# Kernel optimization log

Measured on AMD Instinct MI355X. Metric: run time of the kernel, lower is better.

The kernel has to match this reference:

```python
import jax, jax.numpy as jnp
import numpy as np

N_NODES = 10000
N_EDGES = 640000
D_FEAT = 128


def setup_inputs() -> dict:
    key = jax.random.key(0)
    k1, k2, k3, k4 = jax.random.split(key, 4)
    edge_feat = jax.random.normal(k1, (N_EDGES, D_FEAT), dtype=jnp.float32)
    node_feat = jax.random.normal(k2, (N_NODES, D_FEAT), dtype=jnp.float32)
    recv_idx = jax.random.randint(k3, (N_EDGES,), 0, N_NODES, dtype=jnp.int64 if jax.config.jax_enable_x64 else jnp.int32)
    W = jax.random.normal(k4, (2 * D_FEAT, D_FEAT), dtype=jnp.float32) * (1.0 / np.sqrt(2 * D_FEAT))
    b = jnp.zeros((D_FEAT,), dtype=jnp.float32)
    return {"edge_feat": edge_feat, "node_feat": node_feat, "recv_idx": recv_idx, "W": W, "b": b}


def reference(edge_feat, node_feat, recv_idx, W, b):
    # Unsorted segment sum: scatter-add edge features into receiver nodes. [E,d] -> [N,d]
    n_nodes = node_feat.shape[0]
    agg = jax.ops.segment_sum(edge_feat, recv_idx, num_segments=n_nodes)
    # Concat node features with aggregated received-edge features. [N, 2d]
    collected = jnp.concatenate([node_feat, agg], axis=-1)
    # node_model: Linear(2d -> d)
    return collected @ W + b
```

## Files before the change

### kernel.cpp

```cpp
#include <hip/hip_runtime.h>

#define N_NODES 10000
#define N_EDGES 640000
#define D_FEAT 128

#define WS_COUNTS 0
#define WS_BSUM   10240
#define WS_BOFF   10304
#define WS_START  16384
#define WS_CURSOR 32768
#define WS_SORTED 49152
#define WS_AGG    689152

#define NPB 40

__global__ void zero_counts_kernel(int* __restrict__ counts) {
    int i = blockIdx.x * blockDim.x + threadIdx.x;
    if (i < N_NODES) counts[i] = 0;
}

__global__ void hist_kernel(const int4* __restrict__ recv4, int* __restrict__ counts) {
    int i = blockIdx.x * blockDim.x + threadIdx.x;
    if (i < N_EDGES / 4) {
        const int4 r = recv4[i];
        atomicAdd(&counts[r.x], 1);
        atomicAdd(&counts[r.y], 1);
        atomicAdd(&counts[r.z], 1);
        atomicAdd(&counts[r.w], 1);
    }
}

__global__ __launch_bounds__(256) void prefix1_kernel(const int* __restrict__ counts,
                                                      int* __restrict__ bsum) {
    __shared__ int wsum[4];
    const int tid = threadIdx.x;
    const int idx = blockIdx.x * 256 + tid;
    int x = (idx < N_NODES) ? counts[idx] : 0;
    #pragma unroll
    for (int off = 32; off >= 1; off >>= 1) x += __shfl_down(x, off, 64);
    if ((tid & 63) == 0) wsum[tid >> 6] = x;
    __syncthreads();
    if (tid == 0) bsum[blockIdx.x] = wsum[0] + wsum[1] + wsum[2] + wsum[3];
}

__global__ void prefix2_kernel(const int* __restrict__ bsum,
                               int* __restrict__ boff,
                               int* __restrict__ start) {
    const int lane = threadIdx.x;
    const int v = (lane < NPB) ? bsum[lane] : 0;
    int x = v;
    #pragma unroll
    for (int off = 1; off < 64; off <<= 1) {
        int t = __shfl_up(x, off, 64);
        if (lane >= off) x += t;
    }
    if (lane < NPB) boff[lane] = x - v;
    if (lane == 0) start[N_NODES] = N_EDGES;
}

__global__ __launch_bounds__(256) void prefix3_kernel(const int* __restrict__ counts,
                                                      const int* __restrict__ boff,
                                                      int* __restrict__ start,
                                                      int* __restrict__ cursor) {
    __shared__ int wsum[4];
    const int tid  = threadIdx.x;
    const int idx  = blockIdx.x * 256 + tid;
    const int lane = tid & 63;
    const int wave = tid >> 6;
    const int v = (idx < N_NODES) ? counts[idx] : 0;
    int x = v;
    #pragma unroll
    for (int off = 1; off < 64; off <<= 1) {
        int t = __shfl_up(x, off, 64);
        if (lane >= off) x += t;
    }
    if (lane == 63) wsum[wave] = x;
    __syncthreads();
    int woff = 0;
    #pragma unroll
    for (int k = 0; k < 3; ++k) woff += (k < wave) ? wsum[k] : 0;
    const int excl = boff[blockIdx.x] + woff + x - v;
    if (idx < N_NODES) { start[idx] = excl; cursor[idx] = excl; }
}

__global__ void reorder_kernel(const int4* __restrict__ recv4,
                               int* __restrict__ cursor,
                               int* __restrict__ sorted_eid) {
    int i = blockIdx.x * blockDim.x + threadIdx.x;
    if (i < N_EDGES / 4) {
        const int4 r = recv4[i];
        const int e = i * 4;
        sorted_eid[atomicAdd(&cursor[r.x], 1)] = e + 0;
        sorted_eid[atomicAdd(&cursor[r.y], 1)] = e + 1;
        sorted_eid[atomicAdd(&cursor[r.z], 1)] = e + 2;
        sorted_eid[atomicAdd(&cursor[r.w], 1)] = e + 3;
    }
}

#define GW 16
__global__ __launch_bounds__(512) void gather_kernel(
        const float4* __restrict__ edge_feat4,
        const int* __restrict__ sorted_eid,
        const int* __restrict__ start,
        float4* __restrict__ agg4) {
    __shared__ float4 red[GW][32];
    const int n   = blockIdx.x;
    const int tid = threadIdx.x;
    const int l   = tid & 31;
    const int w   = tid >> 5;
    const int s = start[n];
    const int e = start[n + 1];
    float4 acc = {0.f, 0.f, 0.f, 0.f};
    int i = s + w;
    if (i < e) {
        int eid = sorted_eid[i];
        while (true) {
            const int inext = i + GW;
            const int eid_next = (inext < e) ? sorted_eid[inext] : 0;
            const float4 v = edge_feat4[(long)eid * 32 + l];
            acc.x += v.x; acc.y += v.y; acc.z += v.z; acc.w += v.w;
            i = inext;
            if (i >= e) break;
            eid = eid_next;
        }
    }
    red[w][l] = acc;
    __syncthreads();
    if (w == 0) {
        float4 r = red[0][l];
        #pragma unroll
        for (int g = 1; g < GW; ++g) {
            const float4 t = red[g][l];
            r.x += t.x; r.y += t.y; r.z += t.z; r.w += t.w;
        }
        agg4[(long)n * 32 + l] = r;
    }
}

__global__ __launch_bounds__(256) void gemm_kernel(
        const float* __restrict__ node_feat,
        const float* __restrict__ agg,
        const float* __restrict__ W,
        const float* __restrict__ b,
        float* __restrict__ out) {
    __shared__ __align__(16) float As[32][68];
    __shared__ __align__(16) float Bs[32][64];
    const int tid = threadIdx.x;
    const int tx = tid & 15;
    const int ty = tid >> 4;
    const int m0 = blockIdx.x * 64;
    const int n0 = blockIdx.y * 64;

    float acc[4][4] = {};

    for (int kt = 0; kt < 2 * D_FEAT; kt += 32) {
        const float* src = (kt < D_FEAT) ? (node_feat + kt) : (agg + (kt - D_FEAT));
        {
            const int r  = tid >> 3;
            const int c4 = tid & 7;
            #pragma unroll
            for (int p = 0; p < 2; ++p) {
                int row = m0 + p * 32 + r;
                row = (row < N_NODES) ? row : (N_NODES - 1);
                const float4 a4 = *(const float4*)(src + (long)row * D_FEAT + c4 * 4);
                As[c4 * 4 + 0][p * 32 + r] = a4.x;
                As[c4 * 4 + 1][p * 32 + r] = a4.y;
                As[c4 * 4 + 2][p * 32 + r] = a4.z;
                As[c4 * 4 + 3][p * 32 + r] = a4.w;
            }
        }
        {
            const int r  = tid >> 4;
            const int c4 = tid & 15;
            #pragma unroll
            for (int p = 0; p < 2; ++p) {
                const int row = kt + p * 16 + r;
                *(float4*)&Bs[p * 16 + r][c4 * 4] =
                    *(const float4*)(W + (long)row * D_FEAT + n0 + c4 * 4);
            }
        }
        __syncthreads();
        #pragma unroll
        for (int kk = 0; kk < 32; ++kk) {
            const float4 a4 = *(const float4*)&As[kk][ty * 4];
            const float4 b4 = *(const float4*)&Bs[kk][tx * 4];
            acc[0][0] += a4.x * b4.x; acc[0][1] += a4.x * b4.y;
            acc[0][2] += a4.x * b4.z; acc[0][3] += a4.x * b4.w;
            acc[1][0] += a4.y * b4.x; acc[1][1] += a4.y * b4.y;
            acc[1][2] += a4.y * b4.z; acc[1][3] += a4.y * b4.w;
            acc[2][0] += a4.z * b4.x; acc[2][1] += a4.z * b4.y;
            acc[2][2] += a4.z * b4.z; acc[2][3] += a4.z * b4.w;
            acc[3][0] += a4.w * b4.x; acc[3][1] += a4.w * b4.y;
            acc[3][2] += a4.w * b4.z; acc[3][3] += a4.w * b4.w;
        }
        __syncthreads();
    }

    const float4 bias = *(const float4*)(b + n0 + tx * 4);
    #pragma unroll
    for (int i2 = 0; i2 < 4; ++i2) {
        const int row = m0 + ty * 4 + i2;
        if (row < N_NODES) {
            float4 o;
            o.x = acc[i2][0] + bias.x;
            o.y = acc[i2][1] + bias.y;
            o.z = acc[i2][2] + bias.z;
            o.w = acc[i2][3] + bias.w;
            *(float4*)(out + (long)row * D_FEAT + n0 + tx * 4) = o;
        }
    }
}

extern "C" void kernel_launch(void* const* d_in, const int* in_sizes, int n_in,
                              void* d_out, int out_size, void* d_ws, size_t ws_size,
                              hipStream_t stream) {
    const float* edge_feat = (const float*)d_in[0];
    const float* node_feat = (const float*)d_in[1];
    const int*   recv      = (const int*)d_in[2];
    const float* W         = (const float*)d_in[3];
    const float* b         = (const float*)d_in[4];
    float* out = (float*)d_out;

    int* wsi    = (int*)d_ws;
    int* counts = wsi + WS_COUNTS;
    int* bsum   = wsi + WS_BSUM;
    int* boff   = wsi + WS_BOFF;
    int* startp = wsi + WS_START;
    int* cursor = wsi + WS_CURSOR;
    int* sorted = wsi + WS_SORTED;
    float* agg  = (float*)(wsi + WS_AGG);

    zero_counts_kernel<<<(N_NODES + 255) / 256, 256, 0, stream>>>(counts);
    hist_kernel<<<N_EDGES / 4 / 256, 256, 0, stream>>>((const int4*)recv, counts);
    prefix1_kernel<<<NPB, 256, 0, stream>>>(counts, bsum);
    prefix2_kernel<<<1, 64, 0, stream>>>(bsum, boff, startp);
    prefix3_kernel<<<NPB, 256, 0, stream>>>(counts, boff, startp, cursor);
    reorder_kernel<<<N_EDGES / 4 / 256, 256, 0, stream>>>((const int4*)recv, cursor, sorted);
    gather_kernel<<<N_NODES, 512, 0, stream>>>(
        (const float4*)edge_feat, sorted, startp, (float4*)agg);
    dim3 ggrid((N_NODES + 63) / 64, D_FEAT / 64);
    gemm_kernel<<<ggrid, 256, 0, stream>>>(node_feat, agg, W, b, out);
}
```

Before: 552.3 us.

## Fuse histogram, prefix scan and reorder into one persistent kernel with grid barriers

Replaces six small kernel launches (zero, histogram, three prefix passes, reorder) with a single 256-block persistent kernel. The kernel uses atomic-counter grid barriers between phases, and a memset clears the counts and barrier slots. The goal is to cut launch overhead and inter-kernel gaps. The cost is reliance on all 256 blocks being co-resident to avoid deadlock, and spin-waiting on global atomics at each barrier.

New measurement: 702.3 us. 27.1% more time.

```diff
diff --git a/kernel.cpp b/kernel.cpp
--- a/kernel.cpp
+++ b/kernel.cpp
@@ -4,96 +4,113 @@
 #define N_EDGES 640000
 #define D_FEAT 128
 
+#define SGRID 256
+#define SBLK  512
+#define SNTHREADS (SGRID * SBLK)
+
 #define WS_COUNTS 0
+#define WS_BAR    10016
 #define WS_BSUM   10240
 #define WS_BOFF   10304
+#define WS_CTRL_INTS 10368
 #define WS_START  16384
 #define WS_CURSOR 32768
 #define WS_SORTED 49152
 #define WS_AGG    689152
 
-#define NPB 40
-
-__global__ void zero_counts_kernel(int* __restrict__ counts) {
-    int i = blockIdx.x * blockDim.x + threadIdx.x;
-    if (i < N_NODES) counts[i] = 0;
-}
-
-__global__ void hist_kernel(const int4* __restrict__ recv4, int* __restrict__ counts) {
-    int i = blockIdx.x * blockDim.x + threadIdx.x;
-    if (i < N_EDGES / 4) {
+__device__ __forceinline__ void gbar(int* slot) {
+    __syncthreads();
+    if (threadIdx.x == 0) {
+        __threadfence();
+        atomicAdd(slot, 1);
+        while (atomicAdd(slot, 0) < SGRID) { }
+    }
+    __syncthreads();
+    __threadfence();
+}
+
+__global__ __launch_bounds__(SBLK) void setup_kernel(
+        const int4* __restrict__ recv4,
+        int* __restrict__ ws) {
+    int* counts = ws + WS_COUNTS;
+    int* bar    = ws + WS_BAR;
+    int* bsum   = ws + WS_BSUM;
+    int* boff   = ws + WS_BOFF;
+    int* startp = ws + WS_START;
+    int* cursor = ws + WS_CURSOR;
+    int* sorted = ws + WS_SORTED;
+
+    const int tid  = threadIdx.x;
+    const int bid  = blockIdx.x;
+    const int gtid = bid * SBLK + tid;
+
+    __shared__ int s_wsum[8];
+
+    for (int i = gtid; i < N_EDGES / 4; i += SNTHREADS) {
         const int4 r = recv4[i];
         atomicAdd(&counts[r.x], 1);
         atomicAdd(&counts[r.y], 1);
         atomicAdd(&counts[r.z], 1);
         atomicAdd(&counts[r.w], 1);
     }
-}
-
-__global__ __launch_bounds__(256) void prefix1_kernel(const int* __restrict__ counts,
-                                                      int* __restrict__ bsum) {
-    __shared__ int wsum[4];
-    const int tid = threadIdx.x;
-    const int idx = blockIdx.x * 256 + tid;
-    int x = (idx < N_NODES) ? counts[idx] : 0;
-    #pragma unroll
-    for (int off = 32; off >= 1; off >>= 1) x += __shfl_down(x, off, 64);
-    if ((tid & 63) == 0) wsum[tid >> 6] = x;
-    __syncthreads();
-    if (tid == 0) bsum[blockIdx.x] = wsum[0] + wsum[1] + wsum[2] + wsum[3];
-}
-
-__global__ void prefix2_kernel(const int* __restrict__ bsum,
-                               int* __restrict__ boff,
-                               int* __restrict__ start) {
-    const int lane = threadIdx.x;
-    const int v = (lane < NPB) ? bsum[lane] : 0;
-    int x = v;
-    #pragma unroll
-    for (int off = 1; off < 64; off <<= 1) {
-        int t = __shfl_up(x, off, 64);
-        if (lane >= off) x += t;
-    }
-    if (lane < NPB) boff[lane] = x - v;
-    if (lane == 0) start[N_NODES] = N_EDGES;
-}
-
-__global__ __launch_bounds__(256) void prefix3_kernel(const int* __restrict__ counts,
-                                                      const int* __restrict__ boff,
-                                                      int* __restrict__ start,
-                                                      int* __restrict__ cursor) {
-    __shared__ int wsum[4];
-    const int tid  = threadIdx.x;
-    const int idx  = blockIdx.x * 256 + tid;
-    const int lane = tid & 63;
-    const int wave = tid >> 6;
-    const int v = (idx < N_NODES) ? counts[idx] : 0;
-    int x = v;
-    #pragma unroll
-    for (int off = 1; off < 64; off <<= 1) {
-        int t = __shfl_up(x, off, 64);
-        if (lane >= off) x += t;
-    }
-    if (lane == 63) wsum[wave] = x;
-    __syncthreads();
-    int woff = 0;
-    #pragma unroll
-    for (int k = 0; k < 3; ++k) woff += (k < wave) ? wsum[k] : 0;
-    const int excl = boff[blockIdx.x] + woff + x - v;
-    if (idx < N_NODES) { start[idx] = excl; cursor[idx] = excl; }
-}
-
-__global__ void reorder_kernel(const int4* __restrict__ recv4,
-                               int* __restrict__ cursor,
-                               int* __restrict__ sorted_eid) {
-    int i = blockIdx.x * blockDim.x + threadIdx.x;
-    if (i < N_EDGES / 4) {
+    gbar(&bar[0]);
+
+    if (bid < 40 && tid < 256) {
+        const int idx = bid * 256 + tid;
+        int x = (idx < N_NODES) ? counts[idx] : 0;
+        #pragma unroll
+        for (int off = 32; off >= 1; off >>= 1) x += __shfl_down(x, off, 64);
+        if ((tid & 63) == 0) s_wsum[tid >> 6] = x;
+    }
+    __syncthreads();
+    if (bid < 40 && tid == 0)
+        bsum[bid] = s_wsum[0] + s_wsum[1] + s_wsum[2] + s_wsum[3];
+    gbar(&bar[1]);
+
+    if (bid == 0 && tid < 64) {
+        const int v = (tid < 40) ? bsum[tid] : 0;
+        int x = v;
+        #pragma unroll
+        for (int off = 1; off < 64; off <<= 1) {
+            int t = __shfl_up(x, off, 64);
+            if (tid >= off) x += t;
+        }
+        if (tid < 40) boff[tid] = x - v;
+        if (tid == 0) startp[N_NODES] = N_EDGES;
+    }
+    gbar(&bar[2]);
+
+    int p2_x = 0, p2_v = 0, p2_idx = -1;
+    if (bid < 40 && tid < 256) {
+        p2_idx = bid * 256 + tid;
+        p2_v = (p2_idx < N_NODES) ? counts[p2_idx] : 0;
+        p2_x = p2_v;
+        #pragma unroll
+        for (int off = 1; off < 64; off <<= 1) {
+            int t = __shfl_up(p2_x, off, 64);
+            if ((tid & 63) >= off) p2_x += t;
+        }
+        if ((tid & 63) == 63) s_wsum[4 + (tid >> 6)] = p2_x;
+    }
+    __syncthreads();
+    if (bid < 40 && tid < 256 && p2_idx < N_NODES) {
+        const int wave = tid >> 6;
+        int woff = 0;
+        #pragma unroll
+        for (int k = 0; k < 3; ++k) woff += (k < wave) ? s_wsum[4 + k] : 0;
+        const int excl = boff[bid] + woff + p2_x - p2_v;
+        startp[p2_idx] = excl;
+        cursor[p2_idx] = excl;
+    }
+    gbar(&bar[3]);
+
+    for (int i = gtid; i < N_EDGES / 4; i += SNTHREADS) {
         const int4 r = recv4[i];
         const int e = i * 4;
-        sorted_eid[atomicAdd(&cursor[r.x], 1)] = e + 0;
-        sorted_eid[atomicAdd(&cursor[r.y], 1)] = e + 1;
-        sorted_eid[atomicAdd(&cursor[r.z], 1)] = e + 2;
-        sorted_eid[atomicAdd(&cursor[r.w], 1)] = e + 3;
+        sorted[atomicAdd(&cursor[r.x], 1)] = e + 0;
+        sorted[atomicAdd(&cursor[r.y], 1)] = e + 1;
+        sorted[atomicAdd(&cursor[r.z], 1)] = e + 2;
+        sorted[atomicAdd(&cursor[r.w], 1)] = e + 3;
     }
 }
 
@@ -222,22 +239,17 @@
     float* out = (float*)d_out;
 
     int* wsi    = (int*)d_ws;
-    int* counts = wsi + WS_COUNTS;
-    int* bsum   = wsi + WS_BSUM;
-    int* boff   = wsi + WS_BOFF;
     int* startp = wsi + WS_START;
-    int* cursor = wsi + WS_CURSOR;
     int* sorted = wsi + WS_SORTED;
     float* agg  = (float*)(wsi + WS_AGG);
 
-    zero_counts_kernel<<<(N_NODES + 255) / 256, 256, 0, stream>>>(counts);
-    hist_kernel<<<N_EDGES / 4 / 256, 256, 0, stream>>>((const int4*)recv, counts);
-    prefix1_kernel<<<NPB, 256, 0, stream>>>(counts, bsum);
-    prefix2_kernel<<<1, 64, 0, stream>>>(bsum, boff, startp);
-    prefix3_kernel<<<NPB, 256, 0, stream>>>(counts, boff, startp, cursor);
-    reorder_kernel<<<N_EDGES / 4 / 256, 256, 0, stream>>>((const int4*)recv, cursor, sorted);
+    hipMemsetAsync(d_ws, 0, (size_t)WS_CTRL_INTS * sizeof(int), stream);
+
+    setup_kernel<<<SGRID, SBLK, 0, stream>>>((const int4*)recv, (int*)d_ws);
+
     gather_kernel<<<N_NODES, 512, 0, stream>>>(
         (const float4*)edge_feat, sorted, startp, (float4*)agg);
+
     dim3 ggrid((N_NODES + 63) / 64, D_FEAT / 64);
     gemm_kernel<<<ggrid, 256, 0, stream>>>(node_feat, agg, W, b, out);
 }
```

## Replace global-atomic counting sort with per-block LDS histograms and local cursors

Applied to the files above, without the earlier changes.

The counting sort that groups edges by receiver now runs in 64 blocks. Each block builds a histogram of its edge slice in shared memory and writes it out per block. A per-node scan across the blocks gives each block its own starting offset, and the reorder step then advances cursors with shared-memory atomics instead of global ones. This cuts the kernel launch count and removes global atomic contention, but only 64 blocks run hist and reorder, which may underuse the GPU. Within each block, edge order inside a node is no longer deterministic.

Result: faster. 488.0 us (-11.6%).

```diff
diff --git a/kernel.cpp b/kernel.cpp
--- a/kernel.cpp
+++ b/kernel.cpp
@@ -4,96 +4,103 @@
 #define N_EDGES 640000
 #define D_FEAT 128
 
-#define WS_COUNTS 0
-#define WS_BSUM   10240
-#define WS_BOFF   10304
-#define WS_START  16384
-#define WS_CURSOR 32768
-#define WS_SORTED 49152
-#define WS_AGG    689152
-
-#define NPB 40
-
-__global__ void zero_counts_kernel(int* __restrict__ counts) {
-    int i = blockIdx.x * blockDim.x + threadIdx.x;
-    if (i < N_NODES) counts[i] = 0;
-}
-
-__global__ void hist_kernel(const int4* __restrict__ recv4, int* __restrict__ counts) {
-    int i = blockIdx.x * blockDim.x + threadIdx.x;
-    if (i < N_EDGES / 4) {
-        const int4 r = recv4[i];
-        atomicAdd(&counts[r.x], 1);
-        atomicAdd(&counts[r.y], 1);
-        atomicAdd(&counts[r.z], 1);
-        atomicAdd(&counts[r.w], 1);
-    }
-}
-
-__global__ __launch_bounds__(256) void prefix1_kernel(const int* __restrict__ counts,
-                                                      int* __restrict__ bsum) {
-    __shared__ int wsum[4];
-    const int tid = threadIdx.x;
-    const int idx = blockIdx.x * 256 + tid;
-    int x = (idx < N_NODES) ? counts[idx] : 0;
-    #pragma unroll
-    for (int off = 32; off >= 1; off >>= 1) x += __shfl_down(x, off, 64);
-    if ((tid & 63) == 0) wsum[tid >> 6] = x;
-    __syncthreads();
-    if (tid == 0) bsum[blockIdx.x] = wsum[0] + wsum[1] + wsum[2] + wsum[3];
-}
-
-__global__ void prefix2_kernel(const int* __restrict__ bsum,
-                               int* __restrict__ boff,
-                               int* __restrict__ start) {
-    const int lane = threadIdx.x;
-    const int v = (lane < NPB) ? bsum[lane] : 0;
-    int x = v;
+#define HB   64
+#define HBLK 1024
+#define EPB  (N_EDGES / HB)
+#define BCS  10016
+
+#define WS_BCNT   0
+#define WS_BSUM   641024
+#define WS_START  641088
+#define WS_SORTED 651392
+#define WS_AGG    1291392
+
+__global__ __launch_bounds__(HBLK) void hist_kernel(
+        const int* __restrict__ recv, int* __restrict__ bcnt) {
+    __shared__ int h[N_NODES];
+    for (int i = threadIdx.x; i < N_NODES; i += HBLK) h[i] = 0;
+    __syncthreads();
+    const int4* r4 = (const int4*)(recv + blockIdx.x * EPB);
+    for (int i = threadIdx.x; i < EPB / 4; i += HBLK) {
+        const int4 r = r4[i];
+        atomicAdd(&h[r.x], 1);
+        atomicAdd(&h[r.y], 1);
+        atomicAdd(&h[r.z], 1);
+        atomicAdd(&h[r.w], 1);
+    }
+    __syncthreads();
+    int* dst = bcnt + blockIdx.x * BCS;
+    for (int i = threadIdx.x; i < N_NODES; i += HBLK) dst[i] = h[i];
+}
+
+__global__ __launch_bounds__(256) void scan1_kernel(
+        int* __restrict__ bcnt, int* __restrict__ start, int* __restrict__ bsum) {
+    __shared__ int s_w[4];
+    const int tid = threadIdx.x;
+    const int n   = blockIdx.x * 256 + tid;
+    const bool ok = (n < N_NODES);
+
+    int tot = 0;
+    if (ok) {
+        int run = 0;
+        #pragma unroll
+        for (int b = 0; b < HB; ++b) {
+            int* p = bcnt + b * BCS + n;
+            const int c = *p;
+            *p = run;
+            run += c;
+        }
+        tot = run;
+    }
+    const int lane = tid & 63;
+    const int wave = tid >> 6;
+    int x = tot;
     #pragma unroll
     for (int off = 1; off < 64; off <<= 1) {
         int t = __shfl_up(x, off, 64);
         if (lane >= off) x += t;
     }
-    if (lane < NPB) boff[lane] = x - v;
-    if (lane == 0) start[N_NODES] = N_EDGES;
-}
-
-__global__ __launch_bounds__(256) void prefix3_kernel(const int* __restrict__ counts,
-                                                      const int* __restrict__ boff,
-                                                      int* __restrict__ start,
-                                                      int* __restrict__ cursor) {
-    __shared__ int wsum[4];
-    const int tid  = threadIdx.x;
-    const int idx  = blockIdx.x * 256 + tid;
-    const int lane = tid & 63;
-    const int wave = tid >> 6;
-    const int v = (idx < N_NODES) ? counts[idx] : 0;
-    int x = v;
-    #pragma unroll
-    for (int off = 1; off < 64; off <<= 1) {
-        int t = __shfl_up(x, off, 64);
-        if (lane >= off) x += t;
-    }
-    if (lane == 63) wsum[wave] = x;
+    if (lane == 63) s_w[wave] = x;
     __syncthreads();
     int woff = 0;
     #pragma unroll
-    for (int k = 0; k < 3; ++k) woff += (k < wave) ? wsum[k] : 0;
-    const int excl = boff[blockIdx.x] + woff + x - v;
-    if (idx < N_NODES) { start[idx] = excl; cursor[idx] = excl; }
-}
-
-__global__ void reorder_kernel(const int4* __restrict__ recv4,
-                               int* __restrict__ cursor,
-                               int* __restrict__ sorted_eid) {
-    int i = blockIdx.x * blockDim.x + threadIdx.x;
-    if (i < N_EDGES / 4) {
-        const int4 r = recv4[i];
-        const int e = i * 4;
-        sorted_eid[atomicAdd(&cursor[r.x], 1)] = e + 0;
-        sorted_eid[atomicAdd(&cursor[r.y], 1)] = e + 1;
-        sorted_eid[atomicAdd(&cursor[r.z], 1)] = e + 2;
-        sorted_eid[atomicAdd(&cursor[r.w], 1)] = e + 3;
+    for (int k = 0; k < 3; ++k) woff += (k < wave) ? s_w[k] : 0;
+    if (ok) start[n] = woff + x - tot;
+    if (tid == 0) bsum[blockIdx.x] = s_w[0] + s_w[1] + s_w[2] + s_w[3];
+}
+
+__global__ __launch_bounds__(256) void scan2_kernel(
+        const int* __restrict__ bsum, int* __restrict__ start) {
+    __shared__ int s_boff;
+    const int tid = threadIdx.x;
+    if (tid == 0) {
+        int acc = 0;
+        for (int k = 0; k < (int)blockIdx.x; ++k) acc += bsum[k];
+        s_boff = acc;
+        if (blockIdx.x == 0) start[N_NODES] = N_EDGES;
+    }
+    __syncthreads();
+    const int n = blockIdx.x * 256 + tid;
+    if (n < N_NODES) start[n] += s_boff;
+}
+
+__global__ __launch_bounds__(HBLK) void reorder_kernel(
+        const int* __restrict__ recv, const int* __restrict__ bcnt,
+        const int* __restrict__ start, int* __restrict__ sorted) {
+    __shared__ int cur[N_NODES];
+    const int* rel = bcnt + blockIdx.x * BCS;
+    for (int i = threadIdx.x; i < N_NODES; i += HBLK)
+        cur[i] = start[i] + rel[i];
+    __syncthreads();
+    const int ebase = blockIdx.x * EPB;
+    const int4* r4 = (const int4*)(recv + ebase);
+    for (int i = threadIdx.x; i < EPB / 4; i += HBLK) {
+        const int4 r = r4[i];
+        const int e = ebase + i * 4;
+        sorted[atomicAdd(&cur[r.x], 1)] = e + 0;
+        sorted[atomicAdd(&cur[r.y], 1)] = e + 1;
+        sorted[atomicAdd(&cur[r.z], 1)] = e + 2;
+        sorted[atomicAdd(&cur[r.w], 1)] = e + 3;
     }
 }
 
@@ -222,20 +229,16 @@
     float* out = (float*)d_out;
 
     int* wsi    = (int*)d_ws;
-    int* counts = wsi + WS_COUNTS;
+    int* bcnt   = wsi + WS_BCNT;
     int* bsum   = wsi + WS_BSUM;
-    int* boff   = wsi + WS_BOFF;
     int* startp = wsi + WS_START;
-    int* cursor = wsi + WS_CURSOR;
     int* sorted = wsi + WS_SORTED;
     float* agg  = (float*)(wsi + WS_AGG);
 
-    zero_counts_kernel<<<(N_NODES + 255) / 256, 256, 0, stream>>>(counts);
-    hist_kernel<<<N_EDGES / 4 / 256, 256, 0, stream>>>((const int4*)recv, counts);
-    prefix1_kernel<<<NPB, 256, 0, stream>>>(counts, bsum);
-    prefix2_kernel<<<1, 64, 0, stream>>>(bsum, boff, startp);
-    prefix3_kernel<<<NPB, 256, 0, stream>>>(counts, boff, startp, cursor);
-    reorder_kernel<<<N_EDGES / 4 / 256, 256, 0, stream>>>((const int4*)recv, cursor, sorted);
+    hist_kernel<<<HB, HBLK, 0, stream>>>(recv, bcnt);
+    scan1_kernel<<<(N_NODES + 255) / 256, 256, 0, stream>>>(bcnt, startp, bsum);
+    scan2_kernel<<<(N_NODES + 255) / 256, 256, 0, stream>>>(bsum, startp);
+    reorder_kernel<<<HB, HBLK, 0, stream>>>(recv, bcnt, startp, sorted);
     gather_kernel<<<N_NODES, 512, 0, stream>>>(
         (const float4*)edge_feat, sorted, startp, (float4*)agg);
     dim3 ggrid((N_NODES + 63) / 64, D_FEAT / 64);
```
